# Performance work log

Hardware: AMD Instinct MI355X
Metric: run time of the kernel (lower is better)

## Reference

```python
import jax, jax.numpy as jnp
import numpy as np
from jax import lax

QMAX = 127.0  # qmin=-127, qmax=127 -> 255 LUT entries per axis


def setup_inputs() -> dict:
    key = jax.random.key(0)
    k1, k2, k3 = jax.random.split(key, 3)
    N, C, H, W = 4, 16, 64, 64
    O, KH, KW = 32, 3, 3
    x = jax.random.normal(k1, (N, C, H, W), dtype=jnp.float32)
    weight = jax.random.normal(k2, (O, C, KH, KW), dtype=jnp.float32) * 0.05
    bias = jax.random.normal(k3, (O,), dtype=jnp.float32) * 0.01
    # Approximate-multiplier LUT: lut[i, j] ~= (i-127)*(j-127). Exact product here.
    codes = jnp.arange(-127, 128, dtype=jnp.float32)
    lut = codes[:, None] * codes[None, :]  # [255, 255]
    return {"x": x, "weight": weight, "bias": bias, "lut": lut}


def _quantize_sym(t, scale):
    q = jnp.clip(jnp.round(t / scale), -QMAX, QMAX)
    return q.astype(jnp.int32)


def _lut_conv(x, weight, lut):
    # Symmetric per-tensor quantization of x and w (dynamic abs-max scales).
    scale_x = lax.stop_gradient(jnp.max(jnp.abs(x))) / QMAX
    scale_w = lax.stop_gradient(jnp.max(jnp.abs(weight))) / QMAX
    qx = _quantize_sym(x, scale_x)        # [N,C,H,W] int32 in [-127,127]
    qw = _quantize_sym(weight, scale_w)   # [O,C,KH,KW]

    N, C, H, W = x.shape
    O, _, KH, KW = weight.shape
    ph, pw, sh, sw = 1, 1, 1, 1
    Ho = (H + 2 * ph - KH) // sh + 1
    Wo = (W + 2 * pw - KW) // sw + 1

    px = jnp.pad(qx, ((0, 0), (0, 0), (ph, ph), (pw, pw)))
    rows = (jnp.arange(Ho) * sh)[:, None] + jnp.arange(KH)[None, :]  # [Ho,KH]
    cols = (jnp.arange(Wo) * sw)[:, None] + jnp.arange(KW)[None, :]  # [Wo,KW]
    # Gather patches: [N, C, Ho, Wo, KH, KW]
    patches = px[:, :, rows[:, None, :, None], cols[None, :, None, :]]
    K = C * KH * KW
    # [N, Ho*Wo, C*KH*KW]
    patches = patches.transpose(0, 2, 3, 1, 4, 5).reshape(N, Ho * Wo, K)
    qwf = qw.reshape(O, K)  # [O, K]

    # LUT-based approximate multiply: lut[(qx+127), (qw+127)] then accumulate.
    prod = lut[patches[:, :, None, :] + 127, qwf[None, None, :, :] + 127]  # [N,P,O,K]
    acc = prod.sum(axis=-1)  # [N, P, O]
    y = acc * (scale_x * scale_w)
    return y.transpose(0, 2, 1).reshape(N, O, Ho, Wo)


def reference(x, weight, bias, lut):
    y = _lut_conv(x, weight, lut)
    return y + bias[None, :, None, None]
```

## Files before the change

### kernel.cpp

```cpp
#include <hip/hip_runtime.h>
#include <stdint.h>

#define NB 4
#define CI 16
#define HH 64
#define WW 64
#define OC 32
#define KVOL (CI*3*3)
#define NX (NB*CI*HH*WW)
#define NW (OC*KVOL)
#define QMAXF 127.0f
#define RED_BLOCKS 64

__device__ __forceinline__ int dot4(int a, int b, int c) {
#if __has_builtin(__builtin_amdgcn_sdot4)
  return __builtin_amdgcn_sdot4(a, b, c, false);
#else
  c += ((a << 24) >> 24) * ((b << 24) >> 24);
  c += ((a << 16) >> 24) * ((b << 16) >> 24);
  c += ((a <<  8) >> 24) * ((b <<  8) >> 24);
  c += (a >> 24) * (b >> 24);
  return c;
#endif
}

__global__ __launch_bounds__(256) void reduce_max_kernel(
    const float4* __restrict__ x4, const float4* __restrict__ w4,
    float2* __restrict__ part) {
  float mx = 0.f, mw = 0.f;
  int tid = blockIdx.x * 256 + threadIdx.x;
  #pragma unroll
  for (int k = 0; k < 4; k++) {
    float4 v = x4[tid + k * 16384];
    mx = fmaxf(mx, fmaxf(fmaxf(fabsf(v.x), fabsf(v.y)),
                         fmaxf(fabsf(v.z), fabsf(v.w))));
  }
  if (tid < NW / 4) {
    float4 v = w4[tid];
    mw = fmaxf(mw, fmaxf(fmaxf(fabsf(v.x), fabsf(v.y)),
                         fmaxf(fabsf(v.z), fabsf(v.w))));
  }
  #pragma unroll
  for (int off = 32; off > 0; off >>= 1) {
    mx = fmaxf(mx, __shfl_down(mx, off, 64));
    mw = fmaxf(mw, __shfl_down(mw, off, 64));
  }
  __shared__ float smx[4], smw[4];
  int lane = threadIdx.x & 63, wid = threadIdx.x >> 6;
  if (lane == 0) { smx[wid] = mx; smw[wid] = mw; }
  __syncthreads();
  if (threadIdx.x == 0) {
    part[blockIdx.x] = make_float2(
        fmaxf(fmaxf(smx[0], smx[1]), fmaxf(smx[2], smx[3])),
        fmaxf(fmaxf(smw[0], smw[1]), fmaxf(smw[2], smw[3])));
  }
}

__global__ __launch_bounds__(256) void fused_conv_kernel(
    const float* __restrict__ x, const float* __restrict__ wf,
    const float* __restrict__ bias, const float2* __restrict__ part,
    float* __restrict__ out) {
  __shared__ alignas(16) int8_t qx2[3 * 66 * 20];
  __shared__ alignas(16) int8_t qw2[OC * 9 * 16];

  const int tid = threadIdx.x;
  const int bid = blockIdx.x;
  const int n  = bid >> 6;
  const int ho = bid & 63;

  const int lane = tid & 63;
  float2 pp0 = part[lane];
  float mx = pp0.x, mw = pp0.y;
  #pragma unroll
  for (int off = 32; off > 0; off >>= 1) {
    mx = fmaxf(mx, __shfl_down(mx, off, 64));
    mw = fmaxf(mw, __shfl_down(mw, off, 64));
  }
  mx = __shfl(mx, 0, 64);
  mw = __shfl(mw, 0, 64);
  const float sx = mx / QMAXF;
  const float sw = mw / QMAXF;

  #pragma unroll
  for (int k = 0; k < 18; k++) {
    int i = tid + 256 * k;
    int o = i / 144;
    int r = i - o * 144;
    int c = r / 9;
    int p = r - c * 9;
    float rv = rintf(wf[i] / sw);
    rv = fminf(fmaxf(rv, -QMAXF), QMAXF);
    qw2[(o * 9 + p) * 16 + c] = (int8_t)(int)rv;
  }

  #pragma unroll
  for (int k = 0; k < 12; k++) {
    int i = tid + 256 * k;
    int c  = i / 192;
    int r  = i - c * 192;
    int kh = r >> 6;
    int w  = r & 63;
    int h  = ho - 1 + kh;
    float v = ((unsigned)h < HH) ? x[((n * CI + c) * HH + h) * WW + w] : 0.f;
    float rv = rintf(v / sx);
    rv = fminf(fmaxf(rv, -QMAXF), QMAXF);
    qx2[(kh * 66 + 1 + w) * 20 + c] = (int8_t)(int)rv;
  }
  if (tid < 96) {
    int side = tid & 1;
    int kh = (tid >> 1) % 3;
    int c = tid / 6;
    qx2[(kh * 66 + side * 65) * 20 + c] = 0;
  }
  __syncthreads();

  const int wo = tid & 63;
  const int o0 = (tid >> 6) * 8;
  int acc[8] = {0, 0, 0, 0, 0, 0, 0, 0};

  #pragma unroll
  for (int p = 0; p < 9; p++) {
    const int kh = p / 3, kw = p % 3;
    const int xoff = (kh * 66 + wo + kw) * 20;
    const int woff = (o0 * 9 + p) * 16;
    #pragma unroll
    for (int cq = 0; cq < 4; cq++) {
      const int a = *(const int*)(qx2 + xoff + cq * 4);
      #pragma unroll
      for (int j = 0; j < 8; j++) {
        const int b = *(const int*)(qw2 + woff + j * 144 + cq * 4);
        acc[j] = dot4(a, b, acc[j]);
      }
    }
  }

  const float s = sx * sw;
  #pragma unroll
  for (int j = 0; j < 8; j++) {
    int o = o0 + j;
    out[((n * OC + o) * HH + ho) * WW + wo] = (float)acc[j] * s + bias[o];
  }
}

extern "C" void kernel_launch(void* const* d_in, const int* in_sizes, int n_in,
                              void* d_out, int out_size, void* d_ws, size_t ws_size,
                              hipStream_t stream) {
  const float* x    = (const float*)d_in[0];
  const float* w    = (const float*)d_in[1];
  const float* bias = (const float*)d_in[2];
  float* out = (float*)d_out;
  float2* part = (float2*)d_ws;

  reduce_max_kernel<<<RED_BLOCKS, 256, 0, stream>>>(
      (const float4*)x, (const float4*)w, part);
  fused_conv_kernel<<<NB * HH, 256, 0, stream>>>(x, w, bias, part, out);
}
```

Before: 69.56 us.

## Merge max-reduction and conv into one cooperative kernel with grid sync

The separate abs-max reduction kernel and the conv kernel are replaced by a single cooperative launch of 256 blocks. Each block reduces one slice of x and all of w, then quantizes its own share of the weights into workspace. After a grid-wide sync, every block combines the per-block x maxima and copies the pre-quantized weights into shared memory. This removes one kernel launch and the redundant per-block weight quantization, at the cost of a grid barrier and the constraints of cooperative launch.

```diff
diff --git a/kernel.cpp b/kernel.cpp
--- a/kernel.cpp
+++ b/kernel.cpp
@@ -1,4 +1,5 @@
 #include <hip/hip_runtime.h>
+#include <hip/hip_cooperative_groups.h>
 #include <stdint.h>
 
 #define NB 4
@@ -7,10 +8,8 @@
 #define WW 64
 #define OC 32
 #define KVOL (CI*3*3)
-#define NX (NB*CI*HH*WW)
-#define NW (OC*KVOL)
+#define NWF4 1152
 #define QMAXF 127.0f
-#define RED_BLOCKS 64
 
 __device__ __forceinline__ int dot4(int a, int b, int c) {
 #if __has_builtin(__builtin_amdgcn_sdot4)
@@ -24,78 +23,76 @@
 #endif
 }
 
-__global__ __launch_bounds__(256) void reduce_max_kernel(
-    const float4* __restrict__ x4, const float4* __restrict__ w4,
-    float2* __restrict__ part) {
-  float mx = 0.f, mw = 0.f;
-  int tid = blockIdx.x * 256 + threadIdx.x;
+__global__ __launch_bounds__(256) void fused_all(
+    const float* __restrict__ x, const float* __restrict__ wf,
+    const float* __restrict__ bias, float* __restrict__ ws,
+    float* __restrict__ out) {
+  __shared__ alignas(16) int8_t qx2[3 * 66 * 20];
+  __shared__ alignas(16) int8_t qw2[OC * 9 * 16];
+  __shared__ float sred[8];
+
+  const int tid  = threadIdx.x;
+  const int bid  = blockIdx.x;
+  const int lane = tid & 63, wid = tid >> 6;
+
+  const float4* x4 = (const float4*)x;
+  const float4* w4 = (const float4*)wf;
+  float4 xv = x4[bid * 256 + tid];
+  float mx = fmaxf(fmaxf(fabsf(xv.x), fabsf(xv.y)), fmaxf(fabsf(xv.z), fabsf(xv.w)));
+  float mw = 0.f;
   #pragma unroll
-  for (int k = 0; k < 4; k++) {
-    float4 v = x4[tid + k * 16384];
-    mx = fmaxf(mx, fmaxf(fmaxf(fabsf(v.x), fabsf(v.y)),
-                         fmaxf(fabsf(v.z), fabsf(v.w))));
-  }
-  if (tid < NW / 4) {
-    float4 v = w4[tid];
-    mw = fmaxf(mw, fmaxf(fmaxf(fabsf(v.x), fabsf(v.y)),
-                         fmaxf(fabsf(v.z), fabsf(v.w))));
+  for (int k = 0; k < 5; k++) {
+    int i = tid + 256 * k;
+    if (i < NWF4) {
+      float4 v = w4[i];
+      mw = fmaxf(mw, fmaxf(fmaxf(fabsf(v.x), fabsf(v.y)),
+                           fmaxf(fabsf(v.z), fabsf(v.w))));
+    }
   }
   #pragma unroll
-  for (int off = 32; off > 0; off >>= 1) {
+  for (int off = 32; off; off >>= 1) {
     mx = fmaxf(mx, __shfl_down(mx, off, 64));
     mw = fmaxf(mw, __shfl_down(mw, off, 64));
   }
-  __shared__ float smx[4], smw[4];
-  int lane = threadIdx.x & 63, wid = threadIdx.x >> 6;
-  if (lane == 0) { smx[wid] = mx; smw[wid] = mw; }
+  if (lane == 0) { sred[wid] = mx; sred[4 + wid] = mw; }
   __syncthreads();
-  if (threadIdx.x == 0) {
-    part[blockIdx.x] = make_float2(
-        fmaxf(fmaxf(smx[0], smx[1]), fmaxf(smx[2], smx[3])),
-        fmaxf(fmaxf(smw[0], smw[1]), fmaxf(smw[2], smw[3])));
-  }
-}
+  const float bx = fmaxf(fmaxf(sred[0], sred[1]), fmaxf(sred[2], sred[3]));
+  const float bw = fmaxf(fmaxf(sred[4], sred[5]), fmaxf(sred[6], sred[7]));
+  const float sw = bw / QMAXF;
 
-__global__ __launch_bounds__(256) void fused_conv_kernel(
-    const float* __restrict__ x, const float* __restrict__ wf,
-    const float* __restrict__ bias, const float2* __restrict__ part,
-    float* __restrict__ out) {
-  __shared__ alignas(16) int8_t qx2[3 * 66 * 20];
-  __shared__ alignas(16) int8_t qw2[OC * 9 * 16];
-
-  const int tid = threadIdx.x;
-  const int bid = blockIdx.x;
-  const int n  = bid >> 6;
-  const int ho = bid & 63;
-
-  const int lane = tid & 63;
-  float2 pp0 = part[lane];
-  float mx = pp0.x, mw = pp0.y;
-  #pragma unroll
-  for (int off = 32; off > 0; off >>= 1) {
-    mx = fmaxf(mx, __shfl_down(mx, off, 64));
-    mw = fmaxf(mw, __shfl_down(mw, off, 64));
-  }
-  mx = __shfl(mx, 0, 64);
-  mw = __shfl(mw, 0, 64);
-  const float sx = mx / QMAXF;
-  const float sw = mw / QMAXF;
-
-  #pragma unroll
-  for (int k = 0; k < 18; k++) {
-    int i = tid + 256 * k;
-    int o = i / 144;
-    int r = i - o * 144;
+  float*  part = ws;
+  int8_t* qwg  = (int8_t*)(ws + 256);
+  if (tid == 0) part[bid] = bx;
+  if (tid < 18) {
+    int i = bid * 18 + tid;
+    int o = i / KVOL;
+    int r = i - o * KVOL;
     int c = r / 9;
     int p = r - c * 9;
     float rv = rintf(wf[i] / sw);
     rv = fminf(fmaxf(rv, -QMAXF), QMAXF);
-    qw2[(o * 9 + p) * 16 + c] = (int8_t)(int)rv;
+    qwg[(o * 9 + p) * 16 + c] = (int8_t)(int)rv;
   }
 
+  cooperative_groups::this_grid().sync();
+
+  float gm = 0.f;
+  #pragma unroll
+  for (int k = 0; k < 4; k++) gm = fmaxf(gm, part[k * 64 + lane]);
+  #pragma unroll
+  for (int off = 32; off; off >>= 1) gm = fmaxf(gm, __shfl_down(gm, off, 64));
+  gm = __shfl(gm, 0, 64);
+  const float sx = gm / QMAXF;
+
+  int4* qwl4 = (int4*)qw2;
+  const int4* qwg4 = (const int4*)qwg;
+  qwl4[tid] = qwg4[tid];
+  if (tid < 32) qwl4[256 + tid] = qwg4[256 + tid];
+
+  const int n = bid >> 6, ho = bid & 63;
   #pragma unroll
   for (int k = 0; k < 12; k++) {
-    int i = tid + 256 * k;
+    int i  = tid + 256 * k;
     int c  = i / 192;
     int r  = i - c * 192;
     int kh = r >> 6;
@@ -149,9 +146,8 @@
   const float* w    = (const float*)d_in[1];
   const float* bias = (const float*)d_in[2];
   float* out = (float*)d_out;
-  float2* part = (float2*)d_ws;
+  float* ws  = (float*)d_ws;
 
-  reduce_max_kernel<<<RED_BLOCKS, 256, 0, stream>>>(
-      (const float4*)x, (const float4*)w, part);
-  fused_conv_kernel<<<NB * HH, 256, 0, stream>>>(x, w, bias, part, out);
+  void* args[] = {(void*)&x, (void*)&w, (void*)&bias, (void*)&ws, (void*)&out};
+  hipLaunchCooperativeKernel((void*)fused_all, dim3(256), dim3(256), args, 0, stream);
 }
```

New measurement: 103.0 us. 48.0% more time.
